# Optimization experiments

Hardware: AMD Instinct MI355X
Metric: run time of the kernel (lower is better)

Reference implementation:

```python
import jax, jax.numpy as jnp
import numpy as np

B, NQ, NK, D = 4, 4096, 4096, 256


def setup_inputs() -> dict:
    key = jax.random.key(0)
    ks = jax.random.split(key, 14)
    s = 1.0 / np.sqrt(D)
    def lin(k):
        kw, kb = jax.random.split(k)
        return (jax.random.uniform(kw, (D, D), jnp.float32, -s, s),
                jax.random.uniform(kb, (D,), jnp.float32, -s, s))
    Wq, bq = lin(ks[0]); Wk, bk = lin(ks[1]); Wv, bv = lin(ks[2])
    W1, b1 = lin(ks[3]); W2, b2 = lin(ks[4]); W3, b3 = lin(ks[5])
    x = jax.random.normal(ks[6], (B, NK, D), jnp.float32)
    query = jax.random.normal(ks[7], (B, NQ, D), jnp.float32)
    return {"x": x, "query": query,
            "Wq": Wq, "bq": bq, "Wk": Wk, "bk": bk, "Wv": Wv, "bv": bv,
            "W1": W1, "b1": b1, "W2": W2, "b2": b2, "W3": W3, "b3": b3}


def reference(x, query, Wq, bq, Wk, bk, Wv, bv, W1, b1, W2, b2, W3, b3):
    # Linear: y = x @ W.T + b (torch convention)
    q = jnp.einsum('bnd,ed->bne', query, Wq) + bq   # [B,NQ,D]
    k = jnp.einsum('bnd,ed->bne', x, Wk) + bk       # [B,NK,D]
    v = jnp.einsum('bnd,ed->bne', x, Wv) + bv       # [B,NK,D]
    scale = 1.0 / jnp.sqrt(jnp.float32(x.shape[-1]))
    scores = jnp.einsum('bqd,bkd->bqk', q, k) * scale  # [B,NQ,NK]
    attn = jax.nn.softmax(scores, axis=-1)
    out = jnp.einsum('bqk,bkd->bqd', attn, v)          # [B,NQ,D]
    h = jax.nn.relu(jnp.einsum('bqd,ed->bqe', out, W1) + b1)
    h = jax.nn.relu(jnp.einsum('bqd,ed->bqe', h, W2) + b2)
    h = jax.nn.relu(jnp.einsum('bqd,ed->bqe', h, W3) + b3)
    return h, attn
```

## Files before the change

kernel.cpp:

```cpp
#include <hip/hip_runtime.h>

typedef _Float16 h16;
typedef __attribute__((ext_vector_type(4))) _Float16 h16x4;
typedef __attribute__((ext_vector_type(8))) _Float16 h16x8;
typedef __attribute__((ext_vector_type(4))) float f32x4;

#define NQD 4194304L
#define NROWS 16384L
#define NKK 4096L

static __device__ __forceinline__ f32x4 mfma16(h16x8 a, h16x8 b, f32x4 c) {
  return __builtin_amdgcn_mfma_f32_16x16x32_f16(a, b, c, 0, 0, 0);
}

__global__ void cast_weights(const float* __restrict__ w0, const float* __restrict__ w1,
                             const float* __restrict__ w2, const float* __restrict__ w3,
                             const float* __restrict__ w4, const float* __restrict__ w5,
                             h16* __restrict__ dst) {
  int wi = blockIdx.y;
  const float* src = wi == 0 ? w0 : wi == 1 ? w1 : wi == 2 ? w2 : wi == 3 ? w3 : wi == 4 ? w4 : w5;
  int c = blockIdx.x * 256 + threadIdx.x;
  float4 v = ((const float4*)src)[c];
  h16x4 h = {(h16)v.x, (h16)v.y, (h16)v.z, (h16)v.w};
  *(h16x4*)&dst[(long)wi * 65536 + (long)c * 4] = h;
}

__global__ __launch_bounds__(256) void qkv_proj(const float* __restrict__ x,
                                                const float* __restrict__ qry,
                                                const h16* __restrict__ wh,
                                                const float* __restrict__ bq,
                                                const float* __restrict__ bk,
                                                const float* __restrict__ bv,
                                                h16* __restrict__ qh,
                                                h16* __restrict__ kh,
                                                h16* __restrict__ vT) {
  const int z = blockIdx.z;
  const float* A = (z == 0) ? qry : x;
  const h16* W = wh + (long)z * 65536;
  const float* bias = (z == 0) ? bq : (z == 1) ? bk : bv;
  h16* outH = (z == 0) ? qh : (z == 1) ? kh : nullptr;
  h16* outT = (z == 2) ? vT : nullptr;

  __shared__ h16 smem[128 * 72 + 64 * 72];
  h16 (*As)[72] = (h16(*)[72])smem;
  h16 (*Bs)[72] = (h16(*)[72])(smem + 128 * 72);
  const int tid = threadIdx.x;
  const int wave = tid >> 6, lane = tid & 63;
  const int quad = lane >> 4, l16 = lane & 15;
  const long arow0 = (long)blockIdx.x * 128;
  const int bn = blockIdx.y;
  f32x4 acc[2][4] = {};
  for (int k0 = 0; k0 < 256; k0 += 64) {
    #pragma unroll
    for (int it = 0; it < 8; ++it) {
      int c = it * 256 + tid;
      int r = c >> 4, c4 = (c & 15) * 4;
      float4 v = *(const float4*)&A[(arow0 + r) * 256 + k0 + c4];
      h16x4 h = {(h16)v.x, (h16)v.y, (h16)v.z, (h16)v.w};
      *(h16x4*)&As[r][c4] = h;
    }
    #pragma unroll
    for (int it = 0; it < 2; ++it) {
      int c = it * 256 + tid;
      int r = c >> 3, c8 = (c & 7) * 8;
      *(h16x8*)&Bs[r][c8] = *(const h16x8*)&W[(long)(bn * 64 + r) * 256 + k0 + c8];
    }
    __syncthreads();
    #pragma unroll
    for (int ks = 0; ks < 64; ks += 32) {
      h16x8 a[2], b[4];
      #pragma unroll
      for (int mi = 0; mi < 2; ++mi)
        a[mi] = *(const h16x8*)&As[wave * 32 + mi * 16 + l16][ks + quad * 8];
      #pragma unroll
      for (int ni = 0; ni < 4; ++ni)
        b[ni] = *(const h16x8*)&Bs[ni * 16 + l16][ks + quad * 8];
      #pragma unroll
      for (int mi = 0; mi < 2; ++mi)
        #pragma unroll
        for (int ni = 0; ni < 4; ++ni)
          acc[mi][ni] = mfma16(a[mi], b[ni], acc[mi][ni]);
    }
    __syncthreads();
  }
  if (outH) {
    #pragma unroll
    for (int mi = 0; mi < 2; ++mi) {
      #pragma unroll
      for (int ni = 0; ni < 4; ++ni) {
        int n = bn * 64 + ni * 16 + l16;
        float bv_ = bias[n];
        #pragma unroll
        for (int i = 0; i < 4; ++i) {
          long m = arow0 + wave * 32 + mi * 16 + quad * 4 + i;
          outH[m * 256 + n] = (h16)(acc[mi][ni][i] + bv_);
        }
      }
    }
  } else {
    h16* stg = smem;
    #pragma unroll
    for (int mi = 0; mi < 2; ++mi) {
      #pragma unroll
      for (int ni = 0; ni < 4; ++ni) {
        int dl = ni * 16 + l16;
        float bv_ = bias[bn * 64 + dl];
        int mlb = wave * 32 + mi * 16 + quad * 4;
        h16x4 hv = {(h16)(acc[mi][ni][0] + bv_), (h16)(acc[mi][ni][1] + bv_),
                    (h16)(acc[mi][ni][2] + bv_), (h16)(acc[mi][ni][3] + bv_)};
        *(h16x4*)&stg[dl * 136 + mlb] = hv;
      }
    }
    __syncthreads();
    const int bb = (int)(arow0 >> 12);
    const long kb = arow0 & 4095;
    #pragma unroll
    for (int p = 0; p < 4; ++p) {
      int d = p * 16 + (tid >> 4);
      int c = (tid & 15) * 8;
      h16x8 v = *(const h16x8*)&stg[d * 136 + c];
      *(h16x8*)&outT[((long)bb * 256 + bn * 64 + d) * 4096 + kb + c] = v;
    }
  }
}

__global__ __launch_bounds__(256) void gemm256(const h16* __restrict__ A,
                                               const h16* __restrict__ W,
                                               const float* __restrict__ bias,
                                               h16* __restrict__ outH,
                                               float* __restrict__ outF) {
  __shared__ h16 As[128][72];
  __shared__ h16 Bs[64][72];
  const int tid = threadIdx.x;
  const int wave = tid >> 6, lane = tid & 63;
  const int quad = lane >> 4, l16 = lane & 15;
  const long arow0 = (long)blockIdx.x * 128;
  const int bn = blockIdx.y;
  f32x4 acc[2][4] = {};
  for (int k0 = 0; k0 < 256; k0 += 64) {
    #pragma unroll
    for (int it = 0; it < 4; ++it) {
      int c = it * 256 + tid;
      int r = c >> 3, c8 = (c & 7) * 8;
      *(h16x8*)&As[r][c8] = *(const h16x8*)&A[(arow0 + r) * 256 + k0 + c8];
    }
    #pragma unroll
    for (int it = 0; it < 2; ++it) {
      int c = it * 256 + tid;
      int r = c >> 3, c8 = (c & 7) * 8;
      *(h16x8*)&Bs[r][c8] = *(const h16x8*)&W[(long)(bn * 64 + r) * 256 + k0 + c8];
    }
    __syncthreads();
    #pragma unroll
    for (int ks = 0; ks < 64; ks += 32) {
      h16x8 a[2], b[4];
      #pragma unroll
      for (int mi = 0; mi < 2; ++mi)
        a[mi] = *(const h16x8*)&As[wave * 32 + mi * 16 + l16][ks + quad * 8];
      #pragma unroll
      for (int ni = 0; ni < 4; ++ni)
        b[ni] = *(const h16x8*)&Bs[ni * 16 + l16][ks + quad * 8];
      #pragma unroll
      for (int mi = 0; mi < 2; ++mi)
        #pragma unroll
        for (int ni = 0; ni < 4; ++ni)
          acc[mi][ni] = mfma16(a[mi], b[ni], acc[mi][ni]);
    }
    __syncthreads();
  }
  #pragma unroll
  for (int mi = 0; mi < 2; ++mi) {
    #pragma unroll
    for (int ni = 0; ni < 4; ++ni) {
      int n = bn * 64 + ni * 16 + l16;
      float bv = bias[n];
      #pragma unroll
      for (int i = 0; i < 4; ++i) {
        long m = arow0 + wave * 32 + mi * 16 + quad * 4 + i;
        float v = fmaxf(acc[mi][ni][i] + bv, 0.0f);
        if (outH) outH[m * 256 + n] = (h16)v;
        if (outF) outF[m * 256 + n] = v;
      }
    }
  }
}

__global__ __launch_bounds__(256) void gemm_scores(const h16* __restrict__ qh,
                                                   const h16* __restrict__ kh,
                                                   float2* __restrict__ stats,
                                                   h16* __restrict__ Sh,
                                                   float* __restrict__ Sf) {
  __shared__ h16 smem[128 * 72 * 2];
  h16 (*As)[72] = (h16(*)[72])smem;
  h16 (*Bs)[72] = (h16(*)[72])(smem + 128 * 72);
  const int tid = threadIdx.x;
  const int wave = tid >> 6, lane = tid & 63;
  const int quad = lane >> 4, l16 = lane & 15;
  const int bm = blockIdx.x, bn = blockIdx.y, b = blockIdx.z;
  const h16* Aq = qh + (long)b * 4096 * 256 + (long)bm * 128 * 256;
  const h16* Bk = kh + (long)b * 4096 * 256 + (long)bn * 128 * 256;
  f32x4 acc[2][8] = {};
  for (int k0 = 0; k0 < 256; k0 += 64) {
    #pragma unroll
    for (int it = 0; it < 4; ++it) {
      int c = it * 256 + tid;
      int r = c >> 3, c8 = (c & 7) * 8;
      *(h16x8*)&As[r][c8] = *(const h16x8*)&Aq[(long)r * 256 + k0 + c8];
      *(h16x8*)&Bs[r][c8] = *(const h16x8*)&Bk[(long)r * 256 + k0 + c8];
    }
    __syncthreads();
    #pragma unroll
    for (int ks = 0; ks < 64; ks += 32) {
      h16x8 a[2], bb[8];
      #pragma unroll
      for (int mi = 0; mi < 2; ++mi)
        a[mi] = *(const h16x8*)&As[wave * 32 + mi * 16 + l16][ks + quad * 8];
      #pragma unroll
      for (int ni = 0; ni < 8; ++ni)
        bb[ni] = *(const h16x8*)&Bs[ni * 16 + l16][ks + quad * 8];
      #pragma unroll
      for (int mi = 0; mi < 2; ++mi)
        #pragma unroll
        for (int ni = 0; ni < 8; ++ni)
          acc[mi][ni] = mfma16(a[mi], bb[ni], acc[mi][ni]);
    }
    __syncthreads();
  }
  #pragma unroll
  for (int mi = 0; mi < 2; ++mi)
    #pragma unroll
    for (int ni = 0; ni < 8; ++ni)
      #pragma unroll
      for (int i = 0; i < 4; ++i)
        acc[mi][ni][i] *= 0.0625f;
  #pragma unroll
  for (int mi = 0; mi < 2; ++mi) {
    #pragma unroll
    for (int i = 0; i < 4; ++i) {
      float mx = -1e30f;
      #pragma unroll
      for (int ni = 0; ni < 8; ++ni) mx = fmaxf(mx, acc[mi][ni][i]);
      #pragma unroll
      for (int off = 1; off < 16; off <<= 1) mx = fmaxf(mx, __shfl_xor(mx, off));
      float es = 0.0f;
      #pragma unroll
      for (int ni = 0; ni < 8; ++ni) es += __expf(acc[mi][ni][i] - mx);
      #pragma unroll
      for (int off = 1; off < 16; off <<= 1) es += __shfl_xor(es, off);
      if (l16 == 0) {
        long row = (long)b * 4096 + bm * 128 + wave * 32 + mi * 16 + quad * 4 + i;
        stats[row * 32 + bn] = make_float2(mx, es);
      }
    }
  }
  if (Sh) {
    h16* stg = smem;
    #pragma unroll
    for (int mi = 0; mi < 2; ++mi) {
      #pragma unroll
      for (int ni = 0; ni < 8; ++ni) {
        int c = ni * 16 + l16;
        #pragma unroll
        for (int i = 0; i < 4; ++i) {
          int r = wave * 32 + mi * 16 + quad * 4 + i;
          stg[r * 136 + c] = (h16)acc[mi][ni][i];
        }
      }
    }
    __syncthreads();
    const long rowbase = (long)b * 4096 + (long)bm * 128;
    const long colbase = (long)bn * 128;
    #pragma unroll
    for (int p = 0; p < 8; ++p) {
      int r = p * 16 + (tid >> 4);
      int c = (tid & 15) * 8;
      h16x8 v = *(const h16x8*)&stg[r * 136 + c];
      *(h16x8*)&Sh[(rowbase + r) * 4096 + colbase + c] = v;
    }
  } else {
    #pragma unroll
    for (int mi = 0; mi < 2; ++mi) {
      #pragma unroll
      for (int ni = 0; ni < 8; ++ni) {
        long col = (long)bn * 128 + ni * 16 + l16;
        #pragma unroll
        for (int i = 0; i < 4; ++i) {
          long row = (long)b * 4096 + bm * 128 + wave * 32 + mi * 16 + quad * 4 + i;
          Sf[row * 4096 + col] = acc[mi][ni][i];
        }
      }
    }
  }
}

__global__ __launch_bounds__(256, 4) void gemm_av2(const h16* __restrict__ S,
                                                   const h16* __restrict__ vT,
                                                   const float2* __restrict__ stats,
                                                   float* __restrict__ attn,
                                                   h16* __restrict__ oh) {
  __shared__ h16 As[32][72];
  __shared__ h16 stg[32][136];
  __shared__ float2 rs[32];
  const int tid = threadIdx.x;
  const int wave = tid >> 6, lane = tid & 63;
  const int quad = lane >> 4, l16 = lane & 15;
  const int mb = blockIdx.x, ny = blockIdx.y;
  const long row0 = (long)mb * 32;
  const int b = mb >> 7;
  const h16* Vb = vT + (long)b * 256 * 4096 + ((long)ny * 128) * 4096;

  {
    int r = tid >> 3, j = tid & 7;
    const float2* sp = stats + (row0 + r) * 32 + j * 4;
    float2 sv4[4];
    float m = -1e30f;
    #pragma unroll
    for (int t = 0; t < 4; ++t) { sv4[t] = sp[t]; m = fmaxf(m, sv4[t].x); }
    m = fmaxf(m, __shfl_xor(m, 1));
    m = fmaxf(m, __shfl_xor(m, 2));
    m = fmaxf(m, __shfl_xor(m, 4));
    float e = 0.0f;
    #pragma unroll
    for (int t = 0; t < 4; ++t) e += sv4[t].y * __expf(sv4[t].x - m);
    e += __shfl_xor(e, 1);
    e += __shfl_xor(e, 2);
    e += __shfl_xor(e, 4);
    if (j == 0) rs[r] = make_float2(m, 1.0f / e);
  }
  __syncthreads();

  const int sr = tid >> 3, sc = (tid & 7) * 8;
  const long srow = row0 + sr;
  const float2 st = rs[sr];
  const h16* Srow = S + srow * 4096;
  float* Arow = attn + srow * 4096;

  f32x4 acc[2][2] = {};
  h16x8 sv = *(const h16x8*)&Srow[sc];

  for (int k0 = 0; k0 < 4096; k0 += 64) {
    float p[8];
    #pragma unroll
    for (int e = 0; e < 8; ++e) p[e] = __expf((float)sv[e] - st.x) * st.y;
    if (ny == 0) {
      f32x4 w0 = {p[0], p[1], p[2], p[3]}, w1 = {p[4], p[5], p[6], p[7]};
      __builtin_nontemporal_store(w0, (f32x4*)&Arow[k0 + sc]);
      __builtin_nontemporal_store(w1, (f32x4*)&Arow[k0 + sc + 4]);
    }
    h16x8 ph = {(h16)p[0], (h16)p[1], (h16)p[2], (h16)p[3],
                (h16)p[4], (h16)p[5], (h16)p[6], (h16)p[7]};
    *(h16x8*)&As[sr][sc] = ph;
    h16x8 bb[2][2];
    #pragma unroll
    for (int ks2 = 0; ks2 < 2; ++ks2)
      #pragma unroll
      for (int ni = 0; ni < 2; ++ni)
        bb[ks2][ni] = *(const h16x8*)&Vb[(long)(wave * 32 + ni * 16 + l16) * 4096 + k0 + ks2 * 32 + quad * 8];
    int kn = k0 + 64;
    if (kn < 4096) sv = *(const h16x8*)&Srow[kn + sc];
    __syncthreads();
    #pragma unroll
    for (int ks2 = 0; ks2 < 2; ++ks2) {
      h16x8 a0 = *(const h16x8*)&As[l16][ks2 * 32 + quad * 8];
      h16x8 a1 = *(const h16x8*)&As[16 + l16][ks2 * 32 + quad * 8];
      acc[0][0] = mfma16(a0, bb[ks2][0], acc[0][0]);
      acc[0][1] = mfma16(a0, bb[ks2][1], acc[0][1]);
      acc[1][0] = mfma16(a1, bb[ks2][0], acc[1][0]);
      acc[1][1] = mfma16(a1, bb[ks2][1], acc[1][1]);
    }
    __syncthreads();
  }
  #pragma unroll
  for (int mi = 0; mi < 2; ++mi) {
    #pragma unroll
    for (int ni = 0; ni < 2; ++ni) {
      int col = wave * 32 + ni * 16 + l16;
      #pragma unroll
      for (int i = 0; i < 4; ++i)
        stg[mi * 16 + quad * 4 + i][col] = (h16)acc[mi][ni][i];
    }
  }
  __syncthreads();
  #pragma unroll
  for (int p = 0; p < 2; ++p) {
    int r = tid >> 3;
    int c = (tid & 7) * 8 + p * 64;
    h16x8 v = *(const h16x8*)&stg[r][c];
    *(h16x8*)&oh[(row0 + r) * 256 + ny * 128 + c] = v;
  }
}

template <typename TS>
__global__ __launch_bounds__(512, 2) void gemm_av(const TS* __restrict__ S,
                                                  const h16* __restrict__ vT,
                                                  const float2* __restrict__ stats,
                                                  float* __restrict__ attn,
                                                  h16* __restrict__ oh) {
  __shared__ h16 As[64][72];
  __shared__ h16 Bs[256][72];
  __shared__ float2 rs[64];
  const int tid = threadIdx.x;
  const int wave = tid >> 6, lane = tid & 63;
  const int quad = lane >> 4, l16 = lane & 15;
  const int mb = blockIdx.x;
  const long row0 = (long)mb * 64;
  const int b = mb >> 6;
  const h16* Vb = vT + (long)b * 256 * 4096;

  {
    int r = tid >> 3, j = tid & 7;
    const float2* sp = stats + (row0 + r) * 32 + j * 4;
    float2 sv4[4];
    float m = -1e30f;
    #pragma unroll
    for (int t = 0; t < 4; ++t) { sv4[t] = sp[t]; m = fmaxf(m, sv4[t].x); }
    m = fmaxf(m, __shfl_xor(m, 1));
    m = fmaxf(m, __shfl_xor(m, 2));
    m = fmaxf(m, __shfl_xor(m, 4));
    float e = 0.0f;
    #pragma unroll
    for (int t = 0; t < 4; ++t) e += sv4[t].y * __expf(sv4[t].x - m);
    e += __shfl_xor(e, 1);
    e += __shfl_xor(e, 2);
    e += __shfl_xor(e, 4);
    if (j == 0) rs[r] = make_float2(m, 1.0f / e);
  }
  __syncthreads();

  const int sr = tid >> 3, sc = (tid & 7) * 8;
  const long srow = row0 + sr;
  const float2 st = rs[sr];
  const TS* Srow = S + srow * 4096;
  float* Arow = attn + srow * 4096;
  const int vd = tid >> 3;

  f32x4 acc[4][2] = {};

  h16x8 sv; float4 sa, sb;
  h16x8 bv0, bv1, bv2, bv3;
  if constexpr (sizeof(TS) == 2) {
    sv = *(const h16x8*)&Srow[sc];
  } else {
    sa = *(const float4*)&Srow[sc];
    sb = *(const float4*)&Srow[sc + 4];
  }
  bv0 = *(const h16x8*)&Vb[(long)(vd)       * 4096 + sc];
  bv1 = *(const h16x8*)&Vb[(long)(vd + 64)  * 4096 + sc];
  bv2 = *(const h16x8*)&Vb[(long)(vd + 128) * 4096 + sc];
  bv3 = *(const h16x8*)&Vb[(long)(vd + 192) * 4096 + sc];

  for (int k0 = 0; k0 < 4096; k0 += 64) {
    float p[8];
    if constexpr (sizeof(TS) == 2) {
      #pragma unroll
      for (int e = 0; e < 8; ++e) p[e] = __expf((float)sv[e] - st.x) * st.y;
    } else {
      p[0] = __expf(sa.x - st.x) * st.y; p[1] = __expf(sa.y - st.x) * st.y;
      p[2] = __expf(sa.z - st.x) * st.y; p[3] = __expf(sa.w - st.x) * st.y;
      p[4] = __expf(sb.x - st.x) * st.y; p[5] = __expf(sb.y - st.x) * st.y;
      p[6] = __expf(sb.z - st.x) * st.y; p[7] = __expf(sb.w - st.x) * st.y;
    }
    f32x4 w0 = {p[0], p[1], p[2], p[3]}, w1 = {p[4], p[5], p[6], p[7]};
    __builtin_nontemporal_store(w0, (f32x4*)&Arow[k0 + sc]);
    __builtin_nontemporal_store(w1, (f32x4*)&Arow[k0 + sc + 4]);
    h16x8 ph = {(h16)p[0], (h16)p[1], (h16)p[2], (h16)p[3],
                (h16)p[4], (h16)p[5], (h16)p[6], (h16)p[7]};
    *(h16x8*)&As[sr][sc] = ph;
    *(h16x8*)&Bs[vd][sc]       = bv0;
    *(h16x8*)&Bs[vd + 64][sc]  = bv1;
    *(h16x8*)&Bs[vd + 128][sc] = bv2;
    *(h16x8*)&Bs[vd + 192][sc] = bv3;
    int kn = k0 + 64;
    if (kn < 4096) {
      if constexpr (sizeof(TS) == 2) {
        sv = *(const h16x8*)&Srow[kn + sc];
      } else {
        sa = *(const float4*)&Srow[kn + sc];
        sb = *(const float4*)&Srow[kn + sc + 4];
      }
      bv0 = *(const h16x8*)&Vb[(long)(vd)       * 4096 + kn + sc];
      bv1 = *(const h16x8*)&Vb[(long)(vd + 64)  * 4096 + kn + sc];
      bv2 = *(const h16x8*)&Vb[(long)(vd + 128) * 4096 + kn + sc];
      bv3 = *(const h16x8*)&Vb[(long)(vd + 192) * 4096 + kn + sc];
    }
    __syncthreads();
    #pragma unroll
    for (int ks = 0; ks < 64; ks += 32) {
      h16x8 a[4], bbv[2];
      #pragma unroll
      for (int mi = 0; mi < 4; ++mi)
        a[mi] = *(const h16x8*)&As[mi * 16 + l16][ks + quad * 8];
      #pragma unroll
      for (int ni = 0; ni < 2; ++ni)
        bbv[ni] = *(const h16x8*)&Bs[wave * 32 + ni * 16 + l16][ks + quad * 8];
      #pragma unroll
      for (int mi = 0; mi < 4; ++mi)
        #pragma unroll
        for (int ni = 0; ni < 2; ++ni)
          acc[mi][ni] = mfma16(a[mi], bbv[ni], acc[mi][ni]);
    }
    __syncthreads();
  }
  h16* stg = &Bs[0][0];
  const int SW = 264;
  #pragma unroll
  for (int mi = 0; mi < 4; ++mi) {
    #pragma unroll
    for (int ni = 0; ni < 2; ++ni) {
      int col = wave * 32 + ni * 16 + l16;
      #pragma unroll
      for (int i = 0; i < 4; ++i) {
        int r = mi * 16 + quad * 4 + i;
        stg[r * SW + col] = (h16)acc[mi][ni][i];
      }
    }
  }
  __syncthreads();
  #pragma unroll
  for (int p = 0; p < 4; ++p) {
    int r = tid >> 3;
    int c = (tid & 7) * 8 + p * 64;
    h16x8 v = *(const h16x8*)&stg[r * SW + c];
    *(h16x8*)&oh[(row0 + r) * 256 + c] = v;
  }
}

extern "C" void kernel_launch(void* const* d_in, const int* in_sizes, int n_in,
                              void* d_out, int out_size, void* d_ws, size_t ws_size,
                              hipStream_t stream) {
  (void)in_sizes; (void)n_in; (void)out_size;
  const float* x   = (const float*)d_in[0];
  const float* qry = (const float*)d_in[1];
  const float* Wq  = (const float*)d_in[2];  const float* bq = (const float*)d_in[3];
  const float* Wk  = (const float*)d_in[4];  const float* bk = (const float*)d_in[5];
  const float* Wv  = (const float*)d_in[6];  const float* bv = (const float*)d_in[7];
  const float* W1  = (const float*)d_in[8];  const float* b1 = (const float*)d_in[9];
  const float* W2  = (const float*)d_in[10]; const float* b2 = (const float*)d_in[11];
  const float* W3  = (const float*)d_in[12]; const float* b3 = (const float*)d_in[13];

  float* outH = (float*)d_out;
  float* attn = outH + NQD;

  char* w = (char*)d_ws;
  h16* qh = (h16*)w;
  h16* kh = qh + NQD;
  h16* vT = kh + NQD;
  h16* oh = vT + NQD;
  h16* h1 = oh + NQD;
  h16* h2 = h1 + NQD;
  h16* wh = h2 + NQD;
  size_t off_rs   = (size_t)(6 * NQD + 6 * 65536) * 2;
  size_t BASE     = off_rs + NROWS * 8;
  size_t statsB   = NROWS * 32 * 8;
  size_t ShB      = NROWS * NKK * 2;

  bool modeA = ws_size >= BASE + statsB + ShB;
  bool modeB = !modeA && ws_size >= BASE + statsB;

  float2* stats = (modeA || modeB) ? (float2*)(w + BASE) : (float2*)h1;
  h16*    Sh    = modeA ? (h16*)(w + BASE + statsB) : nullptr;

  cast_weights<<<dim3(64, 6), 256, 0, stream>>>(Wq, Wk, Wv, W1, W2, W3, wh);
  qkv_proj<<<dim3(128, 4, 3), 256, 0, stream>>>(x, qry, wh, bq, bk, bv, qh, kh, vT);
  gemm_scores<<<dim3(32, 32, 4), 256, 0, stream>>>(qh, kh, stats, Sh, modeA ? nullptr : attn);
  if (modeA)
    gemm_av2<<<dim3(512, 2), 256, 0, stream>>>(Sh, vT, stats, attn, oh);
  else
    gemm_av<float><<<dim3(256), 512, 0, stream>>>(attn, vT, stats, attn, oh);
  gemm256<<<dim3(128, 4), 256, 0, stream>>>(oh, wh + 3 * 65536, b1, h1, nullptr);
  gemm256<<<dim3(128, 4), 256, 0, stream>>>(h1, wh + 4 * 65536, b2, h2, nullptr);
  gemm256<<<dim3(128, 4), 256, 0, stream>>>(h2, wh + 5 * 65536, b3, nullptr, outH);
}
```

Measured before the change: 613.8 us.

## Compute full 256-wide AV output per block with LDS-staged V tiles

The attention-times-V kernel previously split the output columns across two blocks. Each of those blocks recomputed the exp of the scores, and each wave loaded its V fragments directly from global memory. Now one block computes all 256 output columns for its 32 rows. V tiles are prefetched into registers, staged through a 256x72 shared buffer, and reused across the M fragments, with eight accumulators per wave. This removes the duplicated exp and S reads, at the cost of more LDS and registers, half as many blocks (occupancy hint lowered to 2), and every block now writing attn.

```diff
diff --git a/kernel.cpp b/kernel.cpp
--- a/kernel.cpp
+++ b/kernel.cpp
@@ -293,21 +293,21 @@
   }
 }
 
-__global__ __launch_bounds__(256, 4) void gemm_av2(const h16* __restrict__ S,
+__global__ __launch_bounds__(256, 2) void gemm_av3(const h16* __restrict__ S,
                                                    const h16* __restrict__ vT,
                                                    const float2* __restrict__ stats,
                                                    float* __restrict__ attn,
                                                    h16* __restrict__ oh) {
   __shared__ h16 As[32][72];
-  __shared__ h16 stg[32][136];
+  __shared__ h16 Bs[256][72];
   __shared__ float2 rs[32];
   const int tid = threadIdx.x;
   const int wave = tid >> 6, lane = tid & 63;
   const int quad = lane >> 4, l16 = lane & 15;
-  const int mb = blockIdx.x, ny = blockIdx.y;
+  const int mb = blockIdx.x;
   const long row0 = (long)mb * 32;
   const int b = mb >> 7;
-  const h16* Vb = vT + (long)b * 256 * 4096 + ((long)ny * 128) * 4096;
+  const h16* Vb = vT + (long)b * 256 * 4096;
 
   {
     int r = tid >> 3, j = tid & 7;
@@ -334,59 +334,73 @@
   const float2 st = rs[sr];
   const h16* Srow = S + srow * 4096;
   float* Arow = attn + srow * 4096;
-
-  f32x4 acc[2][2] = {};
+  const int vr = tid >> 3;
+
+  f32x4 acc[2][4] = {};
+
   h16x8 sv = *(const h16x8*)&Srow[sc];
+  h16x8 bv[8];
+  #pragma unroll
+  for (int p = 0; p < 8; ++p)
+    bv[p] = *(const h16x8*)&Vb[(long)(vr + 32 * p) * 4096 + sc];
 
   for (int k0 = 0; k0 < 4096; k0 += 64) {
     float p[8];
     #pragma unroll
     for (int e = 0; e < 8; ++e) p[e] = __expf((float)sv[e] - st.x) * st.y;
-    if (ny == 0) {
-      f32x4 w0 = {p[0], p[1], p[2], p[3]}, w1 = {p[4], p[5], p[6], p[7]};
-      __builtin_nontemporal_store(w0, (f32x4*)&Arow[k0 + sc]);
-      __builtin_nontemporal_store(w1, (f32x4*)&Arow[k0 + sc + 4]);
-    }
+    f32x4 w0 = {p[0], p[1], p[2], p[3]}, w1 = {p[4], p[5], p[6], p[7]};
+    __builtin_nontemporal_store(w0, (f32x4*)&Arow[k0 + sc]);
+    __builtin_nontemporal_store(w1, (f32x4*)&Arow[k0 + sc + 4]);
     h16x8 ph = {(h16)p[0], (h16)p[1], (h16)p[2], (h16)p[3],
                 (h16)p[4], (h16)p[5], (h16)p[6], (h16)p[7]};
     *(h16x8*)&As[sr][sc] = ph;
-    h16x8 bb[2][2];
-    #pragma unroll
-    for (int ks2 = 0; ks2 < 2; ++ks2)
-      #pragma unroll
-      for (int ni = 0; ni < 2; ++ni)
-        bb[ks2][ni] = *(const h16x8*)&Vb[(long)(wave * 32 + ni * 16 + l16) * 4096 + k0 + ks2 * 32 + quad * 8];
+    #pragma unroll
+    for (int q = 0; q < 8; ++q)
+      *(h16x8*)&Bs[vr + 32 * q][sc] = bv[q];
     int kn = k0 + 64;
-    if (kn < 4096) sv = *(const h16x8*)&Srow[kn + sc];
-    __syncthreads();
-    #pragma unroll
-    for (int ks2 = 0; ks2 < 2; ++ks2) {
-      h16x8 a0 = *(const h16x8*)&As[l16][ks2 * 32 + quad * 8];
-      h16x8 a1 = *(const h16x8*)&As[16 + l16][ks2 * 32 + quad * 8];
-      acc[0][0] = mfma16(a0, bb[ks2][0], acc[0][0]);
-      acc[0][1] = mfma16(a0, bb[ks2][1], acc[0][1]);
-      acc[1][0] = mfma16(a1, bb[ks2][0], acc[1][0]);
-      acc[1][1] = mfma16(a1, bb[ks2][1], acc[1][1]);
-    }
-    __syncthreads();
-  }
+    if (kn < 4096) {
+      sv = *(const h16x8*)&Srow[kn + sc];
+      #pragma unroll
+      for (int q = 0; q < 8; ++q)
+        bv[q] = *(const h16x8*)&Vb[(long)(vr + 32 * q) * 4096 + kn + sc];
+    }
+    __syncthreads();
+    #pragma unroll
+    for (int ks = 0; ks < 64; ks += 32) {
+      h16x8 a[2], bb[4];
+      #pragma unroll
+      for (int mi = 0; mi < 2; ++mi)
+        a[mi] = *(const h16x8*)&As[mi * 16 + l16][ks + quad * 8];
+      #pragma unroll
+      for (int ni = 0; ni < 4; ++ni)
+        bb[ni] = *(const h16x8*)&Bs[wave * 64 + ni * 16 + l16][ks + quad * 8];
+      #pragma unroll
+      for (int mi = 0; mi < 2; ++mi)
+        #pragma unroll
+        for (int ni = 0; ni < 4; ++ni)
+          acc[mi][ni] = mfma16(a[mi], bb[ni], acc[mi][ni]);
+    }
+    __syncthreads();
+  }
+  h16* stg = &Bs[0][0];
+  const int SW = 264;
   #pragma unroll
   for (int mi = 0; mi < 2; ++mi) {
     #pragma unroll
-    for (int ni = 0; ni < 2; ++ni) {
-      int col = wave * 32 + ni * 16 + l16;
+    for (int ni = 0; ni < 4; ++ni) {
+      int col = wave * 64 + ni * 16 + l16;
       #pragma unroll
       for (int i = 0; i < 4; ++i)
-        stg[mi * 16 + quad * 4 + i][col] = (h16)acc[mi][ni][i];
+        stg[(mi * 16 + quad * 4 + i) * SW + col] = (h16)acc[mi][ni][i];
     }
   }
   __syncthreads();
   #pragma unroll
-  for (int p = 0; p < 2; ++p) {
+  for (int p = 0; p < 4; ++p) {
     int r = tid >> 3;
     int c = (tid & 7) * 8 + p * 64;
-    h16x8 v = *(const h16x8*)&stg[r][c];
-    *(h16x8*)&oh[(row0 + r) * 256 + ny * 128 + c] = v;
+    h16x8 v = *(const h16x8*)&stg[r * SW + c];
+    *(h16x8*)&oh[(row0 + r) * 256 + c] = v;
   }
 }
 
@@ -564,7 +578,7 @@
   qkv_proj<<<dim3(128, 4, 3), 256, 0, stream>>>(x, qry, wh, bq, bk, bv, qh, kh, vT);
   gemm_scores<<<dim3(32, 32, 4), 256, 0, stream>>>(qh, kh, stats, Sh, modeA ? nullptr : attn);
   if (modeA)
-    gemm_av2<<<dim3(512, 2), 256, 0, stream>>>(Sh, vT, stats, attn, oh);
+    gemm_av3<<<dim3(512), 256, 0, stream>>>(Sh, vT, stats, attn, oh);
   else
     gemm_av<float><<<dim3(256), 512, 0, stream>>>(attn, vT, stats, attn, oh);
   gemm256<<<dim3(128, 4), 256, 0, stream>>>(oh, wh + 3 * 65536, b1, h1, nullptr);
```

New measurement: 540.0 us. -12.0%, faster.
